# Performance work log

Hardware: AMD Instinct MI355X
Metric: run time of the kernel (lower is better)

Reference implementation:

```python
import jax, jax.numpy as jnp
import numpy as np

C_SIZE = 512
STRIDE = 4
OUT = C_SIZE // STRIDE          # 128, density grid side
GRID = OUT * OUT                # 16384
REG = 10.0
ITERS = 100                     # num_of_iter_in_ot
M_EPS = 1e-16
B = 8                           # batch of images
N = 1024                        # points per image (fixed for jit; ragged in torch)


def setup_inputs() -> dict:
    key = jax.random.key(0)
    k1, k2 = jax.random.split(key, 2)
    d = jax.random.uniform(k1, (B, 1, OUT, OUT), dtype=jnp.float32)
    # normed_density sums to 1 per image (a probability map), unnormed is raw density
    normed_density = d / jnp.sum(d, axis=(1, 2, 3), keepdims=True)
    unnormed_density = d * 100.0
    points = jax.random.uniform(k2, (B, N, 2), dtype=jnp.float32) * C_SIZE
    gt_discrete = jnp.zeros((B, 1, OUT, OUT), dtype=jnp.float32)
    return {"normed_density": normed_density, "unnormed_density": unnormed_density,
            "points": points, "gt_discrete": gt_discrete}


def _per_image(nd, und, pts):
    # nd, und: (1, OUT, OUT); pts: (N, 2)
    cood = jnp.arange(0, C_SIZE, STRIDE, dtype=jnp.float32) + STRIDE / 2.0  # (OUT,)
    x = pts[:, 0:1]
    y = pts[:, 1:2]
    # squared-distance decomposition: -2*x*c + x^2 + c^2
    x_dis = x * x - 2.0 * x * cood[None, :] + cood[None, :] ** 2  # (N, OUT)
    y_dis = y * y - 2.0 * y * cood[None, :] + cood[None, :] ** 2  # (N, OUT)
    dis = (y_dis[:, :, None] + x_dis[:, None, :]).reshape(N, GRID)  # (N, GRID)

    a = jnp.full((N,), 1.0 / N, dtype=jnp.float32)          # target_prob (points)
    b = jax.lax.stop_gradient(nd.reshape(-1))               # source_prob (density, detached)
    K = jnp.exp(-dis / REG)                                 # (N, GRID) Gibbs kernel

    def step(carry, _):
        u, v = carry
        v = b / (u @ K + M_EPS)      # K^T u
        u = a / (K @ v + M_EPS)
        return (u, v), None

    u0 = jnp.full((N,), 1.0 / N, dtype=jnp.float32)
    v0 = jnp.full((GRID,), 1.0 / GRID, dtype=jnp.float32)
    (u, v), _ = jax.lax.scan(step, (u0, v0), None, length=ITERS)

    P = u[:, None] * K * v[None, :]                          # transport plan (N, GRID)
    beta = jax.lax.stop_gradient(REG * jnp.log(v + M_EPS))   # source dual potential

    ot_obj = jnp.sum(nd.reshape(-1) * beta)
    sd = jax.lax.stop_gradient(und.reshape(-1))              # source_density (detached)
    sc = sd.sum()
    denom = sc * sc + 1e-8
    im_grad = (sc / denom) * beta - (sd * beta).sum() / denom  # detached in torch
    loss = jnp.sum(und.reshape(-1) * im_grad)
    wd = jax.lax.stop_gradient(jnp.sum(dis * P))              # .item() in torch
    return loss, wd, ot_obj


def reference(normed_density, unnormed_density, points, gt_discrete):
    losses, wds, ots = jax.vmap(_per_image)(normed_density, unnormed_density, points)
    # torch returns (loss, wd, ot_obj_values); packed as a (3,) array here
    return jnp.stack([losses.sum(), wds.sum(), ots.sum()])
```

## Files before the change

### kernel.cpp

```cpp
#include <hip/hip_runtime.h>


#define N_IMG   8
#define N_PTS   1024
#define OUT_D   128
#define N_CELLS (OUT_D * OUT_D)
#define WIN     11
#define RT      5
#define WINX    14
#define N_TILE  1024
#define N_CHUNK 16
#define CAPE    32768
#define EPS     1e-16f
#define INV_N   (1.0f / 1024.0f)
#define N_ITERS 100

typedef unsigned int   uint_t;
typedef unsigned short u16;
typedef float v2f __attribute__((ext_vector_type(2)));

__device__ __forceinline__ u16 f2bf(float f) {
    uint_t b = __float_as_uint(f);
    b += 0x7FFFu + ((b >> 16) & 1u);
    return (u16)(b >> 16);
}
__device__ __forceinline__ float bflo(uint_t w){ return __uint_as_float(w << 16); }
__device__ __forceinline__ float bfhi(uint_t w){ return __uint_as_float(w & 0xFFFF0000u); }

__global__ __launch_bounds__(1024) void ot_build(
    const float* __restrict__ pts, uint4* __restrict__ cstream,
    u16* __restrict__ pstream, u16* __restrict__ tileofg,
    uint_t* __restrict__ cbaseg, uint_t* __restrict__ cleng)
{
    __shared__ uint_t chist[N_CELLS];
    __shared__ u16    P[128 * 129];
    __shared__ u16    c0tab[N_PTS];
    __shared__ u16    tslot[N_TILE];
    __shared__ u16    tlen[N_TILE];
    __shared__ u16    tof[N_TILE];
    __shared__ uint_t bins[1025];
    __shared__ uint_t cbase_l[N_CHUNK + 1];

    const int img = blockIdx.x, tid = threadIdx.x;
    for (int i = tid; i < N_CELLS; i += 1024) chist[i] = 0;
    for (int i = tid; i < 1025;    i += 1024) bins[i] = 0;
    __syncthreads();

    const float x = pts[(img * N_PTS + tid) * 2 + 0];
    const float y = pts[(img * N_PTS + tid) * 2 + 1];
    const int nx = (int)floorf((x - 2.f) * 0.25f + 0.5f);
    const int ny = (int)floorf((y - 2.f) * 0.25f + 0.5f);
    const int ix0 = min(max(nx - RT, 0), OUT_D - WIN);
    const int iy0 = min(max(ny - RT, 0), OUT_D - WIN);
    const float xx = x * x, yy = y * y;
    float kx[WIN], ky[WIN];
#pragma unroll
    for (int k = 0; k < WIN; ++k) {
        float cx = (float)(4 * (ix0 + k) + 2);
        kx[k] = __expf(-((xx - 2.f * x * cx) + cx * cx) * 0.1f);
        float cy = (float)(4 * (iy0 + k) + 2);
        ky[k] = __expf(-((yy - 2.f * y * cy) + cy * cy) * 0.1f);
    }
    const int cell0 = (iy0 << 7) | ix0;
    c0tab[tid] = (u16)cell0;
    atomicAdd(&chist[cell0], 1u);
    __syncthreads();

    if (tid < 128) {
        uint_t acc = 0;
        P[tid * 129 + 0] = 0;
        for (int c = 0; c < 128; ++c) { acc += chist[(tid << 7) + c]; P[tid * 129 + c + 1] = (u16)acc; }
    }
    __syncthreads();

    int rank = 0;
    for (int p = 0; p < N_PTS; ++p) rank += (p < tid && c0tab[p] == (u16)cell0) ? 1 : 0;

    {
        int ty = tid >> 5, tx = tid & 31;
        int rlo = max(4 * ty - 10, 0), rhi = min(4 * ty + 3, OUT_D - WIN);
        int xlo = max(4 * tx - 10, 0), xhi = min(4 * tx + 3, OUT_D - WIN);
        uint_t len = 0;
        for (int r = rlo; r <= rhi; ++r)
            len += (uint_t)P[r * 129 + xhi + 1] - (uint_t)P[r * 129 + xlo];
        tlen[tid] = (u16)len;
        atomicAdd(&bins[len], 1u);
    }
    __syncthreads();
    if (tid == 0) {
        uint_t acc = 0;
        for (int L = 1024; L >= 0; --L) { uint_t t = bins[L]; bins[L] = acc; acc += t; }
    }
    __syncthreads();
    {
        uint_t slot = atomicAdd(&bins[tlen[tid]], 1u);
        tslot[tid] = (u16)slot;
        tof[slot] = (u16)tid;
    }
    __syncthreads();
    if (tid < N_CHUNK) cbase_l[tid] = tlen[tof[tid * 64]];
    __syncthreads();
    if (tid == 0) {
        uint_t acc = 0;
        for (int c = 0; c < N_CHUNK; ++c) { uint_t l = cbase_l[c]; cbase_l[c] = acc; acc += l * 64u; }
        cbase_l[N_CHUNK] = acc;
    }
    __syncthreads();
    tileofg[img * N_TILE + tid] = tof[tid];
    if (tid < N_CHUNK) {
        cbaseg[img * N_CHUNK + tid] = cbase_l[tid];
        cleng[img * N_CHUNK + tid]  = tlen[tof[tid * 64]];
    }

    uint4* cs = cstream + (size_t)img * CAPE;
    u16*   ps = pstream + (size_t)img * CAPE;
    const int tya = iy0 >> 2, tyb = (iy0 + 10) >> 2;
    const int txa = ix0 >> 2, txb = (ix0 + 10) >> 2;
    for (int ty = tya; ty <= tyb; ++ty) {
        for (int tx = txa; tx <= txb; ++tx) {
            int ti = (ty << 5) | tx;
            int slot = tslot[ti];
            int xlo = max(4 * tx - 10, 0), xhi = min(4 * tx + 3, OUT_D - WIN);
            int rlo = max(4 * ty - 10, 0);
            uint_t idx = (uint_t)rank + (uint_t)P[iy0 * 129 + ix0] - (uint_t)P[iy0 * 129 + xlo];
            for (int r = rlo; r < iy0; ++r)
                idx += (uint_t)P[r * 129 + xhi + 1] - (uint_t)P[r * 129 + xlo];
            uint_t eofs = cbase_l[slot >> 6] + idx * 64u + (uint_t)(slot & 63);
            if (eofs < CAPE) {
                u16 kxp[4], kyp[4];
#pragma unroll
                for (int c = 0; c < 4; ++c) {
                    int dk = 4 * tx + c - ix0;
                    kxp[c] = ((unsigned)dk < 11u) ? f2bf(kx[dk]) : (u16)0;
                    int dj = 4 * ty + c - iy0;
                    kyp[c] = ((unsigned)dj < 11u) ? f2bf(ky[dj]) : (u16)0;
                }
                cs[eofs] = make_uint4((uint_t)kxp[0] | ((uint_t)kxp[1] << 16),
                                      (uint_t)kxp[2] | ((uint_t)kxp[3] << 16),
                                      (uint_t)kyp[0] | ((uint_t)kyp[1] << 16),
                                      (uint_t)kyp[2] | ((uint_t)kyp[3] << 16));
                ps[eofs] = (u16)tid;
            }
        }
    }
}

__device__ __forceinline__ float blk_sum(float v, volatile float* red)
{
#pragma unroll
    for (int o = 32; o; o >>= 1) v += __shfl_xor(v, o, 64);
    int wave = threadIdx.x >> 6, lane = threadIdx.x & 63;
    if (lane == 0) red[wave] = v;
    __syncthreads();
    if (threadIdx.x < 64) {
        float t = (lane < 16) ? red[lane] : 0.0f;
#pragma unroll
        for (int o = 8; o; o >>= 1) t += __shfl_xor(t, o, 64);
        if (lane == 0) red[0] = t;
    }
    __syncthreads();
    float r = red[0];
    __syncthreads();
    return r;
}

__global__ __launch_bounds__(1024) void ot_fused(
    const float* __restrict__ nd, const float* __restrict__ und,
    const float* __restrict__ pts, const uint4* __restrict__ cstream,
    const u16* __restrict__ pstream, const u16* __restrict__ tileofg,
    const uint_t* __restrict__ cbaseg, const uint_t* __restrict__ cleng,
    float* __restrict__ parts)
{
    __shared__ __align__(16) float V[N_CELLS + 16];
    __shared__ float  su[N_PTS];
    __shared__ uint_t cbase_l[N_CHUNK];
    __shared__ uint_t clen_l[N_CHUNK];
    __shared__ float  red[64];

    const int img = blockIdx.x, tid = threadIdx.x;
    const int w = tid >> 6, lane = tid & 63;
    const float* ndi = nd + img * N_CELLS;

    if (tid < N_CHUNK) { cbase_l[tid] = cbaseg[img * N_CHUNK + tid]; clen_l[tid] = cleng[img * N_CHUNK + tid]; }
    if (tid < 16) V[N_CELLS + tid] = 0.0f;
    su[tid] = INV_N;
    __syncthreads();

    const int tile = (int)tileofg[img * N_TILE + w * 64 + lane];
    const int ty4 = (tile >> 5) * 4, tx4 = (tile & 31) * 4;
    float4 b4[4];
#pragma unroll
    for (int r = 0; r < 4; ++r) b4[r] = *(const float4*)(ndi + (ty4 + r) * OUT_D + tx4);
    const uint4* csb = cstream + (size_t)img * CAPE + cbase_l[w] + lane;
    const u16*   psb = pstream + (size_t)img * CAPE + cbase_l[w] + lane;
    const int    alen = (int)clen_l[w];

    const float x = pts[(img * N_PTS + tid) * 2 + 0];
    const float y = pts[(img * N_PTS + tid) * 2 + 1];
    const int nx = (int)floorf((x - 2.f) * 0.25f + 0.5f);
    const int ny = (int)floorf((y - 2.f) * 0.25f + 0.5f);
    const int ix0 = min(max(nx - RT, 0), OUT_D - WIN);
    const int iy0 = min(max(ny - RT, 0), OUT_D - WIN);
    const int ixq = ix0 & ~3;
    const float xx = x * x, yy = y * y;
    v2f kx2[WINX / 2], ky2[WIN];
#pragma unroll
    for (int d = 0; d < WINX; ++d) {
        int col = ixq + d, dk = col - ix0;
        float cx = (float)(4 * col + 2);
        float kv = ((unsigned)dk < 11u) ? __expf(-((xx - 2.f * x * cx) + cx * cx) * 0.1f) : 0.f;
        kx2[d >> 1][d & 1] = kv;
    }
#pragma unroll
    for (int j = 0; j < WIN; ++j) {
        float cy = (float)(4 * (iy0 + j) + 2);
        float kv = __expf(-((yy - 2.f * y * cy) + cy * cy) * 0.1f);
        ky2[j] = (v2f){kv, kv};
    }
    float ureg = INV_N;
    const float* vbp = &V[iy0 * OUT_D + ixq];

    for (int it = 0; it < N_ITERS; ++it) {
        v2f acc2[8] = {};
        uint4 cw = make_uint4(0u, 0u, 0u, 0u); u16 pid = 0;
        if (alen > 0) { cw = csb[0]; pid = psb[0]; }
        for (int t = 1; t <= alen; ++t) {
            uint4 cwn = csb[(size_t)t * 64];
            u16   pn  = psb[(size_t)t * 64];
            float uv = su[pid & 1023u];
            v2f kxa = {bflo(cw.x), bfhi(cw.x)};
            v2f kxb = {bflo(cw.y), bfhi(cw.y)};
            float u0 = uv * bflo(cw.z), u1 = uv * bfhi(cw.z);
            float u2 = uv * bflo(cw.w), u3 = uv * bfhi(cw.w);
            v2f s0 = {u0, u0}, s1 = {u1, u1}, s2 = {u2, u2}, s3 = {u3, u3};
            acc2[0] += s0 * kxa;  acc2[1] += s0 * kxb;
            acc2[2] += s1 * kxa;  acc2[3] += s1 * kxb;
            acc2[4] += s2 * kxa;  acc2[5] += s2 * kxb;
            acc2[6] += s3 * kxa;  acc2[7] += s3 * kxb;
            cw = cwn; pid = pn;
        }
#pragma unroll
        for (int r = 0; r < 4; ++r) {
            float4 o;
            o.x = b4[r].x * __builtin_amdgcn_rcpf(acc2[2 * r][0] + EPS);
            o.y = b4[r].y * __builtin_amdgcn_rcpf(acc2[2 * r][1] + EPS);
            o.z = b4[r].z * __builtin_amdgcn_rcpf(acc2[2 * r + 1][0] + EPS);
            o.w = b4[r].w * __builtin_amdgcn_rcpf(acc2[2 * r + 1][1] + EPS);
            *(float4*)&V[(ty4 + r) * OUT_D + tx4] = o;
        }
        __syncthreads();

        v2f t2 = {0.f, 0.f};
#pragma unroll
        for (int j = 0; j < WIN; ++j) {
            const float* row = vbp + j * OUT_D;
            float4 va = *(const float4*)(row);
            float4 vb = *(const float4*)(row + 4);
            float4 vc = *(const float4*)(row + 8);
            v2f    vd = *(const v2f*)(row + 12);
            v2f rs;
            rs  = kx2[0] * (v2f){va.x, va.y};
            rs += kx2[1] * (v2f){va.z, va.w};
            rs += kx2[2] * (v2f){vb.x, vb.y};
            rs += kx2[3] * (v2f){vb.z, vb.w};
            rs += kx2[4] * (v2f){vc.x, vc.y};
            rs += kx2[5] * (v2f){vc.z, vc.w};
            rs += kx2[6] * vd;
            t2 += ky2[j] * rs;
        }
        float tt = t2.x + t2.y;
        ureg = INV_N / (tt + EPS);
        su[tid] = ureg;
        __syncthreads();
    }

    const float* sdi = und + img * N_CELLS;
    float sc = 0.f, T = 0.f, ot = 0.f;
#pragma unroll
    for (int r = 0; r < 16; ++r) {
        int c = r * 1024 + tid;
        float beta = 10.0f * logf(V[c] + EPS);
        float s = sdi[c];
        sc += s;
        T  = fmaf(s, beta, T);
        ot = fmaf(ndi[c], beta, ot);
    }
    sc = blk_sum(sc, red);
    T  = blk_sum(T,  red);
    ot = blk_sum(ot, red);
    float denom = sc * sc + 1e-8f;
    float c1 = sc / denom, c2 = T / denom;

    float loss = 0.f;
#pragma unroll
    for (int r = 0; r < 16; ++r) {
        int c = r * 1024 + tid;
        float beta = 10.0f * logf(V[c] + EPS);
        loss = fmaf(sdi[c], fmaf(c1, beta, -c2), loss);
    }
    loss = blk_sum(loss, red);

    float wd = 0.f;
#pragma unroll
    for (int j = 0; j < WIN; ++j) {
        float cy = (float)(4 * (iy0 + j) + 2);
        float dy = (yy - 2.f * y * cy) + cy * cy;
        const float* row = vbp + j * OUT_D;
        float skv = 0.f, sdkv = 0.f;
#pragma unroll
        for (int d = 0; d < WINX; ++d) {
            float cx = (float)(4 * (ixq + d) + 2);
            float dx = (xx - 2.f * x * cx) + cx * cx;
            float kv = kx2[d >> 1][d & 1] * row[d];
            skv += kv;
            sdkv = fmaf(dx, kv, sdkv);
        }
        wd = fmaf(ky2[j][0], fmaf(dy, skv, sdkv), wd);
    }
    wd *= ureg;
    wd = blk_sum(wd, red);

    if (tid == 0) {
        parts[img * 3 + 0] = loss;
        parts[img * 3 + 1] = wd;
        parts[img * 3 + 2] = ot;
    }
}

__global__ void ot_sum(const float* __restrict__ parts, float* __restrict__ out)
{
    int t = threadIdx.x;
    if (t < 3) {
        float s = 0.f;
        for (int i = 0; i < N_IMG; ++i) s += parts[i * 3 + t];
        out[t] = s;
    }
}

extern "C" void kernel_launch(void* const* d_in, const int* in_sizes, int n_in,
                              void* d_out, int out_size, void* d_ws, size_t ws_size,
                              hipStream_t stream_)
{
    const float* nd  = (const float*)d_in[0];
    const float* und = (const float*)d_in[1];
    const float* pts = (const float*)d_in[2];

    char* ws = (char*)d_ws;
    uint4*  cstream = (uint4*)ws;
    u16*    pstream = (u16*)(ws + 4194304);
    u16*    tileofg = (u16*)(ws + 4718592);
    uint_t* cbaseg  = (uint_t*)(ws + 4734976);
    uint_t* cleng   = (uint_t*)(ws + 4735488);
    float*  parts   = (float*)(ws + 4736000);

    hipMemsetAsync(cstream, 0, 4194304, stream_);
    ot_build<<<N_IMG, 1024, 0, stream_>>>(pts, cstream, pstream, tileofg, cbaseg, cleng);
    ot_fused<<<N_IMG, 1024, 0, stream_>>>(nd, und, pts, cstream, pstream, tileofg,
                                          cbaseg, cleng, parts);
    ot_sum<<<1, 64, 0, stream_>>>(parts, (float*)d_out);
}
```

Baseline: 846.3 us.

## Reorder points by x-bank bucket and unroll streamed K^T u loop

Points are bucketed by the LDS bank offset of their window start column, sorted once in shared memory, and assigned to threads in an interleaved order. The aim is for lanes in a wave to read V rows from different banks during the K·v update, cutting LDS bank conflicts; u is now written back at the permuted index. The compressed-stream accumulation loop is also unrolled by four with a deeper prefetch of stream words, to hide global load latency. The cost is a one-time O(N) per-thread ranking pass, more registers for the prefetched values, and unconditional loads of the first four stream entries.

Result: slower. 943.1 us (+11.4%).

```diff
diff --git a/kernel.cpp b/kernel.cpp
--- a/kernel.cpp
+++ b/kernel.cpp
@@ -173,6 +173,9 @@
 {
     __shared__ __align__(16) float V[N_CELLS + 16];
     __shared__ float  su[N_PTS];
+    __shared__ u16    bktab[N_PTS];
+    __shared__ u16    sorted_pt[N_PTS];
+    __shared__ uint_t xhist[8];
     __shared__ uint_t cbase_l[N_CHUNK];
     __shared__ uint_t clen_l[N_CHUNK];
     __shared__ float  red[64];
@@ -183,8 +186,33 @@
 
     if (tid < N_CHUNK) { cbase_l[tid] = cbaseg[img * N_CHUNK + tid]; clen_l[tid] = cleng[img * N_CHUNK + tid]; }
     if (tid < 16) V[N_CELLS + tid] = 0.0f;
+    if (tid < 8)  xhist[tid] = 0;
     su[tid] = INV_N;
     __syncthreads();
+
+    {
+        float x_ = pts[(img * N_PTS + tid) * 2 + 0];
+        int nx_ = (int)floorf((x_ - 2.f) * 0.25f + 0.5f);
+        int i0_ = min(max(nx_ - RT, 0), OUT_D - WIN);
+        bktab[tid] = (u16)(((i0_ & ~3) >> 2) & 7);
+    }
+    __syncthreads();
+    {
+        int bkt = (int)bktab[tid];
+        int rnk = 0;
+        for (int p = 0; p < N_PTS; ++p)
+            rnk += (p < tid && (int)bktab[p] == bkt) ? 1 : 0;
+        atomicAdd(&xhist[bkt], 1u);
+        __syncthreads();
+        if (tid == 0) {
+            uint_t acc = 0;
+            for (int b = 0; b < 8; ++b) { uint_t t = xhist[b]; xhist[b] = acc; acc += t; }
+        }
+        __syncthreads();
+        sorted_pt[xhist[bkt] + rnk] = (u16)tid;
+    }
+    __syncthreads();
+    const int pp = (int)sorted_pt[((tid & 7) << 7) | (tid >> 3)];
 
     const int tile = (int)tileofg[img * N_TILE + w * 64 + lane];
     const int ty4 = (tile >> 5) * 4, tx4 = (tile & 31) * 4;
@@ -195,8 +223,8 @@
     const u16*   psb = pstream + (size_t)img * CAPE + cbase_l[w] + lane;
     const int    alen = (int)clen_l[w];
 
-    const float x = pts[(img * N_PTS + tid) * 2 + 0];
-    const float y = pts[(img * N_PTS + tid) * 2 + 1];
+    const float x = pts[(img * N_PTS + pp) * 2 + 0];
+    const float y = pts[(img * N_PTS + pp) * 2 + 1];
     const int nx = (int)floorf((x - 2.f) * 0.25f + 0.5f);
     const int ny = (int)floorf((y - 2.f) * 0.25f + 0.5f);
     const int ix0 = min(max(nx - RT, 0), OUT_D - WIN);
@@ -222,23 +250,38 @@
 
     for (int it = 0; it < N_ITERS; ++it) {
         v2f acc2[8] = {};
-        uint4 cw = make_uint4(0u, 0u, 0u, 0u); u16 pid = 0;
-        if (alen > 0) { cw = csb[0]; pid = psb[0]; }
-        for (int t = 1; t <= alen; ++t) {
-            uint4 cwn = csb[(size_t)t * 64];
-            u16   pn  = psb[(size_t)t * 64];
-            float uv = su[pid & 1023u];
+        auto PROC = [&](const uint4 cw, uint_t pidv) {
+            float uvv = su[pidv & 1023u];
             v2f kxa = {bflo(cw.x), bfhi(cw.x)};
             v2f kxb = {bflo(cw.y), bfhi(cw.y)};
-            float u0 = uv * bflo(cw.z), u1 = uv * bfhi(cw.z);
-            float u2 = uv * bflo(cw.w), u3 = uv * bfhi(cw.w);
+            float u0 = uvv * bflo(cw.z), u1 = uvv * bfhi(cw.z);
+            float u2 = uvv * bflo(cw.w), u3 = uvv * bfhi(cw.w);
             v2f s0 = {u0, u0}, s1 = {u1, u1}, s2 = {u2, u2}, s3 = {u3, u3};
             acc2[0] += s0 * kxa;  acc2[1] += s0 * kxb;
             acc2[2] += s1 * kxa;  acc2[3] += s1 * kxb;
             acc2[4] += s2 * kxa;  acc2[5] += s2 * kxb;
             acc2[6] += s3 * kxa;  acc2[7] += s3 * kxb;
-            cw = cwn; pid = pn;
-        }
+        };
+        uint4 c0 = csb[0],   c1 = csb[64],  c2 = csb[128], c3 = csb[192];
+        u16   p0 = psb[0],   p1 = psb[64],  p2 = psb[128], p3 = psb[192];
+        int t = 0;
+        for (; t + 8 <= alen; t += 4) {
+            uint4 n0 = csb[(size_t)(t + 4) * 64], n1 = csb[(size_t)(t + 5) * 64];
+            uint4 n2 = csb[(size_t)(t + 6) * 64], n3 = csb[(size_t)(t + 7) * 64];
+            u16   q0 = psb[(size_t)(t + 4) * 64], q1 = psb[(size_t)(t + 5) * 64];
+            u16   q2 = psb[(size_t)(t + 6) * 64], q3 = psb[(size_t)(t + 7) * 64];
+            PROC(c0, p0); PROC(c1, p1); PROC(c2, p2); PROC(c3, p3);
+            c0 = n0; c1 = n1; c2 = n2; c3 = n3;
+            p0 = q0; p1 = q1; p2 = q2; p3 = q3;
+        }
+        int rr = alen - t;
+        if (rr > 0) PROC(c0, p0);
+        if (rr > 1) PROC(c1, p1);
+        if (rr > 2) PROC(c2, p2);
+        if (rr > 3) PROC(c3, p3);
+        for (int s = t + 4; s < alen; ++s)
+            PROC(csb[(size_t)s * 64], psb[(size_t)s * 64]);
+
 #pragma unroll
         for (int r = 0; r < 4; ++r) {
             float4 o;
@@ -270,7 +313,7 @@
         }
         float tt = t2.x + t2.y;
         ureg = INV_N / (tt + EPS);
-        su[tid] = ureg;
+        su[pp] = ureg;
         __syncthreads();
     }
 
```
